# Kernel tuning notes

Measured on AMD Instinct MI355X. Metric: run time of the kernel, lower is better.

The kernel has to match this reference:

```python
import jax, jax.numpy as jnp
import numpy as np

N = 50000        # nodes
E = 800000       # directed edges (before self-loops)
F_IN = 128       # num_features
GAT_DIM = 16     # per-head channels
HEADS = 4
HID = GAT_DIM * HEADS   # 64, concat output of each GATConv
FC = 10 * GAT_DIM       # 160
OUT = 64                # output_dim
NEG_SLOPE = 0.2         # PyG GATConv default


def _gat_conv(x, W, a_src, a_dst, b, src, dst):
    """One PyG-style GATConv (concat=True, self-loops already in src/dst).
    x: [N, Fin], W: [Fin, HEADS*GAT_DIM], a_src/a_dst: [HEADS, GAT_DIM], b: [HEADS*GAT_DIM]."""
    H, C = a_src.shape
    h = (x @ W).reshape(N, H, C)                       # [N,H,C]
    s_src = (h * a_src).sum(-1)                        # [N,H] per-node src score
    s_dst = (h * a_dst).sum(-1)                        # [N,H]
    e = jax.nn.leaky_relu(s_src[src] + s_dst[dst], NEG_SLOPE)  # [Etot,H]
    # segment softmax over incoming edges of each destination node
    m = jax.ops.segment_max(e, dst, num_segments=N)    # [N,H]
    ex = jnp.exp(e - m[dst])
    z = jax.ops.segment_sum(ex, dst, num_segments=N)   # [N,H]
    alpha = ex / (z[dst] + 1e-16)                      # [Etot,H]
    msg = h[src] * alpha[:, :, None]                   # [Etot,H,C]
    out = jax.ops.segment_sum(msg, dst, num_segments=N)
    return out.reshape(N, H * C) + b


def setup_inputs() -> dict:
    key = jax.random.key(0)
    ks = jax.random.split(key, 20)
    sc = 0.05
    inp = {
        "x": jax.random.normal(ks[0], (N, F_IN), dtype=jnp.float32),
        "edge_index": jax.random.randint(ks[1], (2, E), 0, N, dtype=jnp.int32),
        "W0": jax.random.normal(ks[2], (F_IN, HID), dtype=jnp.float32) * sc,
        "as0": jax.random.normal(ks[3], (HEADS, GAT_DIM), dtype=jnp.float32) * sc,
        "ad0": jax.random.normal(ks[4], (HEADS, GAT_DIM), dtype=jnp.float32) * sc,
        "b0": jnp.zeros((HID,), jnp.float32),
        "W1": jax.random.normal(ks[5], (HID, HID), dtype=jnp.float32) * sc,
        "as1": jax.random.normal(ks[6], (HEADS, GAT_DIM), dtype=jnp.float32) * sc,
        "ad1": jax.random.normal(ks[7], (HEADS, GAT_DIM), dtype=jnp.float32) * sc,
        "b1": jnp.zeros((HID,), jnp.float32),
        "W2": jax.random.normal(ks[8], (HID, HID), dtype=jnp.float32) * sc,
        "as2": jax.random.normal(ks[9], (HEADS, GAT_DIM), dtype=jnp.float32) * sc,
        "ad2": jax.random.normal(ks[10], (HEADS, GAT_DIM), dtype=jnp.float32) * sc,
        "b2": jnp.zeros((HID,), jnp.float32),
        "fw1": jax.random.normal(ks[11], (HID, FC), dtype=jnp.float32) * sc,
        "fb1": jnp.zeros((FC,), jnp.float32),
        "fw2": jax.random.normal(ks[12], (FC, OUT), dtype=jnp.float32) * sc,
        "fb2": jnp.zeros((OUT,), jnp.float32),
    }
    return inp


def reference(x, edge_index, W0, as0, ad0, b0, W1, as1, ad1, b1, W2, as2, ad2, b2, fw1, fb1, fw2, fb2):
    loop = jnp.arange(N, dtype=edge_index.dtype)
    src = jnp.concatenate([edge_index[0], loop])   # PyG add_self_loops=True
    dst = jnp.concatenate([edge_index[1], loop])
    h = jax.nn.relu(_gat_conv(x, W0, as0, ad0, b0, src, dst))
    h = jax.nn.relu(_gat_conv(h, W1, as1, ad1, b1, src, dst))
    h = jax.nn.relu(_gat_conv(h, W2, as2, ad2, b2, src, dst))
    h = jax.nn.relu(h @ fw1 + fb1)
    return h @ fw2 + fb2
```

## Files before the change

kernel.cpp:

```cpp
#include <hip/hip_runtime.h>
#include <hip/hip_fp16.h>

#define NN 50000
#define EE 800000
#define ETOT (EE + NN)
#define HIDD 64
#define NHEADS 4
#define FCD 160
#define OUTD 64

#define NBKT 196
#define BSTRIDE 5120
#define CHUNK 4096
#define NEBLK ((ETOT + CHUNK - 1) / CHUNK)
#define NGB   ((NN + 63) / 64)
#define NFC128 ((NN + 127) / 128)


__global__ void k_zero(int* __restrict__ cursor) {
    int t = threadIdx.x;
    if (t < NBKT) cursor[t] = 0;
}

__global__ __launch_bounds__(256) void k_binwrite(const int* __restrict__ ei,
                                                  int* __restrict__ cursor,
                                                  unsigned* __restrict__ binned) {
    __shared__ int hist[NBKT];
    __shared__ int sbase[NBKT];
    __shared__ int cur[NBKT];
    int t = threadIdx.x;
    for (int i = t; i < NBKT; i += 256) hist[i] = 0;
    __syncthreads();
    int base = blockIdx.x * CHUNK;
    for (int k = t; k < CHUNK; k += 256) {
        int i = base + k;
        if (i < ETOT) {
            int dst = (i < EE) ? ei[EE + i] : (i - EE);
            atomicAdd(&hist[dst >> 8], 1);
        }
    }
    __syncthreads();
    for (int b = t; b < NBKT; b += 256) {
        int c = hist[b];
        sbase[b] = b * BSTRIDE + (c ? atomicAdd(&cursor[b], c) : 0);
        cur[b] = 0;
    }
    __syncthreads();
    for (int k = t; k < CHUNK; k += 256) {
        int i = base + k;
        if (i < ETOT) {
            int src, dst;
            if (i < EE) { src = ei[i]; dst = ei[EE + i]; }
            else { src = dst = i - EE; }
            int b = dst >> 8;
            int p = atomicAdd(&cur[b], 1);
            binned[sbase[b] + p] = ((unsigned)src << 8) | (unsigned)(dst & 255);
        }
    }
}

__global__ __launch_bounds__(256) void k_csr_final(const int* __restrict__ cursor,
                                                   const unsigned* __restrict__ binned,
                                                   int* __restrict__ rowbeg,
                                                   int* __restrict__ rowend,
                                                   int* __restrict__ csrc) {
    __shared__ int hist[256];
    __shared__ int cur[256];
    __shared__ int wsum[4];
    int b = blockIdx.x;
    int t = threadIdx.x;
    int s0 = b * BSTRIDE;
    int cnt = cursor[b];
    hist[t] = 0;
    __syncthreads();
    for (int k = t; k < cnt; k += 256) {
        unsigned pr = binned[s0 + k];
        atomicAdd(&hist[pr & 255u], 1);
    }
    __syncthreads();
    int v = hist[t];
    int lane = t & 63, w = t >> 6;
    int x = v;
    #pragma unroll
    for (int off = 1; off < 64; off <<= 1) {
        int y = __shfl_up(x, off);
        if (lane >= off) x += y;
    }
    if (lane == 63) wsum[w] = x;
    __syncthreads();
    int add = 0;
    #pragma unroll
    for (int k = 0; k < 4; k++) add += (k < w) ? wsum[k] : 0;
    int excl = x + add - v;
    int n = (b << 8) + t;
    if (n < NN) {
        rowbeg[n] = s0 + excl;
        rowend[n] = s0 + excl + v;
    }
    cur[t] = s0 + excl;
    __syncthreads();
    for (int k = t; k < cnt; k += 256) {
        unsigned pr = binned[s0 + k];
        int p = atomicAdd(&cur[pr & 255u], 1);
        csrc[p] = (int)(pr >> 8);
    }
}


template<int FIN>
__global__ __launch_bounds__(256) void k_gemm_scores(
        const float* __restrict__ x, const float* __restrict__ W,
        const float* __restrict__ a_src, const float* __restrict__ a_dst,
        __half* __restrict__ h, float* __restrict__ ssrc, float* __restrict__ sdst) {
    __shared__ float wl[64 * 64];
    __shared__ float xt[64][68];
    int t = threadIdx.x;
    int nb = blockIdx.x * 64;
    int qg = t & 15, ng = t >> 4;
    float acc[4][4] = {};
    const float4* wl4 = (const float4*)wl;

    #pragma unroll
    for (int p = 0; p < FIN / 64; p++) {
        if (p) __syncthreads();
        for (int i = t; i < 64 * 64 / 4; i += 256)
            ((float4*)wl)[i] = ((const float4*)W)[p * 1024 + i];
        #pragma unroll
        for (int r = 0; r < 4; r++) {
            int idx = t + r * 256;
            int node = idx & 63, kq = idx >> 6;
            int n = nb + node;
            float4 v = make_float4(0.f, 0.f, 0.f, 0.f);
            if (n < NN) v = *(const float4*)(x + (size_t)n * FIN + p * 64 + kq * 4);
            xt[kq * 4 + 0][node] = v.x;
            xt[kq * 4 + 1][node] = v.y;
            xt[kq * 4 + 2][node] = v.z;
            xt[kq * 4 + 3][node] = v.w;
        }
        __syncthreads();
        #pragma unroll 4
        for (int k = 0; k < 64; k++) {
            float4 wv = wl4[k * 16 + qg];
            float4 xv = *(const float4*)&xt[k][ng * 4];
            acc[0][0] += xv.x * wv.x; acc[0][1] += xv.x * wv.y;
            acc[0][2] += xv.x * wv.z; acc[0][3] += xv.x * wv.w;
            acc[1][0] += xv.y * wv.x; acc[1][1] += xv.y * wv.y;
            acc[1][2] += xv.y * wv.z; acc[1][3] += xv.y * wv.w;
            acc[2][0] += xv.z * wv.x; acc[2][1] += xv.z * wv.y;
            acc[2][2] += xv.z * wv.z; acc[2][3] += xv.z * wv.w;
            acc[3][0] += xv.w * wv.x; acc[3][1] += xv.w * wv.y;
            acc[3][2] += xv.w * wv.z; acc[3][3] += xv.w * wv.w;
        }
    }

    #pragma unroll
    for (int r = 0; r < 4; r++) {
        int n = nb + ng * 4 + r;
        if (n < NN) {
            union { __half2 h2[2]; uint2 u; } pk;
            pk.h2[0] = __floats2half2_rn(acc[r][0], acc[r][1]);
            pk.h2[1] = __floats2half2_rn(acc[r][2], acc[r][3]);
            *(uint2*)(h + (size_t)n * HIDD + qg * 4) = pk.u;
        }
    }

    float as0 = a_src[qg * 4 + 0], as1 = a_src[qg * 4 + 1];
    float as2 = a_src[qg * 4 + 2], as3 = a_src[qg * 4 + 3];
    float ad0 = a_dst[qg * 4 + 0], ad1 = a_dst[qg * 4 + 1];
    float ad2 = a_dst[qg * 4 + 2], ad3 = a_dst[qg * 4 + 3];
    float vs[4], vd[4];
    #pragma unroll
    for (int r = 0; r < 4; r++) {
        vs[r] = acc[r][0] * as0 + acc[r][1] * as1 + acc[r][2] * as2 + acc[r][3] * as3;
        vd[r] = acc[r][0] * ad0 + acc[r][1] * ad1 + acc[r][2] * ad2 + acc[r][3] * ad3;
        vs[r] += __shfl_xor(vs[r], 1); vs[r] += __shfl_xor(vs[r], 2);
        vd[r] += __shfl_xor(vd[r], 1); vd[r] += __shfl_xor(vd[r], 2);
    }
    if ((qg & 3) == 0) {
        int hd = qg >> 2;
        #pragma unroll
        for (int r = 0; r < 4; r++) {
            int n = nb + ng * 4 + r;
            if (n < NN) {
                ssrc[n * NHEADS + hd] = vs[r];
                sdst[n * NHEADS + hd] = vd[r];
            }
        }
    }
}


__global__ __launch_bounds__(512) void k_aggr_gemm(
        const __half* __restrict__ h, const float* __restrict__ ssrc,
        const float* __restrict__ sdst, const int* __restrict__ rowbeg,
        const int* __restrict__ rowend, const int* __restrict__ csrc,
        const float* __restrict__ bias, const float* __restrict__ W,
        const float* __restrict__ a_src, const float* __restrict__ a_dst,
        __half* __restrict__ hout, float* __restrict__ ssrc_o,
        float* __restrict__ sdst_o) {
    __shared__ float wl[64 * 64];
    __shared__ float xt[64][68];
    int t = threadIdx.x;
    int nb = blockIdx.x * 64;

    for (int i = t; i < 64 * 64 / 4; i += 512)
        ((float4*)wl)[i] = ((const float4*)W)[i];

    {
        int wid = t >> 6, lane = t & 63;
        int sub = lane >> 4, c4 = lane & 15, hd = c4 >> 2;
        #pragma unroll 1
        for (int i = 0; i < 8; i++) {
            int nl = wid * 8 + i;
            int n = nb + nl;
            float4 acc = make_float4(0.f, 0.f, 0.f, 0.f);
            float z = 0.f;
            if (n < NN) {
                int beg = rowbeg[n], end = rowend[n];
                float sdh = sdst[n * NHEADS + hd];
                for (int cb = beg; cb < end; cb += 64) {
                    int m = min(64, end - cb);
                    int s_all = (cb + lane < end) ? csrc[cb + lane] : 0;
                    for (int pb = 0; pb < m; pb += 16) {
                        float ssv[4]; uint2 hr[4];
                        #pragma unroll
                        for (int o = 0; o < 4; o++) {
                            int jj = pb + sub * 4 + o;
                            int s = __shfl(s_all, jj);
                            if (jj < m) {
                                ssv[o] = ssrc[s * NHEADS + hd];
                                hr[o] = *(const uint2*)(h + (size_t)s * HIDD + c4 * 4);
                            }
                        }
                        #pragma unroll
                        for (int o = 0; o < 4; o++) {
                            int jj = pb + sub * 4 + o;
                            if (jj < m) {
                                float eh = ssv[o] + sdh;
                                eh = eh > 0.f ? eh : 0.2f * eh;
                                float w = __expf(eh);
                                float2 lo = __half22float2(*(__half2*)&hr[o].x);
                                float2 hi = __half22float2(*(__half2*)&hr[o].y);
                                acc.x += lo.x * w; acc.y += lo.y * w;
                                acc.z += hi.x * w; acc.w += hi.y * w;
                                z += w;
                            }
                        }
                    }
                }
            }
            acc.x += __shfl_xor(acc.x, 16); acc.y += __shfl_xor(acc.y, 16);
            acc.z += __shfl_xor(acc.z, 16); acc.w += __shfl_xor(acc.w, 16);
            z += __shfl_xor(z, 16);
            acc.x += __shfl_xor(acc.x, 32); acc.y += __shfl_xor(acc.y, 32);
            acc.z += __shfl_xor(acc.z, 32); acc.w += __shfl_xor(acc.w, 32);
            z += __shfl_xor(z, 32);
            if (sub == 0) {
                float inv_z = 1.0f / (z + 1e-16f);
                float4 bv = *(const float4*)(bias + c4 * 4);
                float v0 = acc.x * inv_z + bv.x; v0 = v0 > 0.f ? v0 : 0.f;
                float v1 = acc.y * inv_z + bv.y; v1 = v1 > 0.f ? v1 : 0.f;
                float v2 = acc.z * inv_z + bv.z; v2 = v2 > 0.f ? v2 : 0.f;
                float v3 = acc.w * inv_z + bv.w; v3 = v3 > 0.f ? v3 : 0.f;
                if (n >= NN) { v0 = v1 = v2 = v3 = 0.f; }
                xt[c4 * 4 + 0][nl] = v0;
                xt[c4 * 4 + 1][nl] = v1;
                xt[c4 * 4 + 2][nl] = v2;
                xt[c4 * 4 + 3][nl] = v3;
            }
        }
    }
    __syncthreads();

    {
        int qg = t & 15, ng = t >> 4;
        float acc[2][4] = {};
        const float4* wl4 = (const float4*)wl;
        #pragma unroll 4
        for (int k = 0; k < 64; k++) {
            float4 wv = wl4[k * 16 + qg];
            float2 xv = *(const float2*)&xt[k][ng * 2];
            acc[0][0] += xv.x * wv.x; acc[0][1] += xv.x * wv.y;
            acc[0][2] += xv.x * wv.z; acc[0][3] += xv.x * wv.w;
            acc[1][0] += xv.y * wv.x; acc[1][1] += xv.y * wv.y;
            acc[1][2] += xv.y * wv.z; acc[1][3] += xv.y * wv.w;
        }
        #pragma unroll
        for (int r = 0; r < 2; r++) {
            int n = nb + ng * 2 + r;
            if (n < NN) {
                union { __half2 h2[2]; uint2 u; } pk;
                pk.h2[0] = __floats2half2_rn(acc[r][0], acc[r][1]);
                pk.h2[1] = __floats2half2_rn(acc[r][2], acc[r][3]);
                *(uint2*)(hout + (size_t)n * HIDD + qg * 4) = pk.u;
            }
        }
        float as0 = a_src[qg * 4 + 0], as1 = a_src[qg * 4 + 1];
        float as2 = a_src[qg * 4 + 2], as3 = a_src[qg * 4 + 3];
        float ad0 = a_dst[qg * 4 + 0], ad1 = a_dst[qg * 4 + 1];
        float ad2 = a_dst[qg * 4 + 2], ad3 = a_dst[qg * 4 + 3];
        float vs[2], vd[2];
        #pragma unroll
        for (int r = 0; r < 2; r++) {
            vs[r] = acc[r][0] * as0 + acc[r][1] * as1 + acc[r][2] * as2 + acc[r][3] * as3;
            vd[r] = acc[r][0] * ad0 + acc[r][1] * ad1 + acc[r][2] * ad2 + acc[r][3] * ad3;
            vs[r] += __shfl_xor(vs[r], 1); vs[r] += __shfl_xor(vs[r], 2);
            vd[r] += __shfl_xor(vd[r], 1); vd[r] += __shfl_xor(vd[r], 2);
        }
        if ((qg & 3) == 0) {
            int hd = qg >> 2;
            #pragma unroll
            for (int r = 0; r < 2; r++) {
                int n = nb + ng * 2 + r;
                if (n < NN) {
                    ssrc_o[n * NHEADS + hd] = vs[r];
                    sdst_o[n * NHEADS + hd] = vd[r];
                }
            }
        }
    }
}


__global__ __launch_bounds__(256) void k_aggr(
        const __half* __restrict__ h, const float* __restrict__ ssrc,
        const float* __restrict__ sdst, const int* __restrict__ rowbeg,
        const int* __restrict__ rowend,
        const int* __restrict__ csrc, const float* __restrict__ bias,
        __half* __restrict__ out) {
    int wid  = threadIdx.x >> 6;
    int lane = threadIdx.x & 63;
    int n = blockIdx.x * 4 + wid;
    int sub = lane >> 4;
    int c4  = lane & 15;
    int hd  = c4 >> 2;
    int beg = rowbeg[n], end = rowend[n];
    float sdh = sdst[n * NHEADS + hd];

    float4 acc = make_float4(0.f, 0.f, 0.f, 0.f);
    float z = 0.f;
    for (int cb = beg; cb < end; cb += 64) {
        int m = min(64, end - cb);
        int s_all = (cb + lane < end) ? csrc[cb + lane] : 0;
        for (int pb = 0; pb < m; pb += 16) {
            float ssv[4]; uint2 hr[4];
            #pragma unroll
            for (int o = 0; o < 4; o++) {
                int jj = pb + sub * 4 + o;
                int s = __shfl(s_all, jj);
                if (jj < m) {
                    ssv[o] = ssrc[s * NHEADS + hd];
                    hr[o] = *(const uint2*)(h + (size_t)s * HIDD + c4 * 4);
                }
            }
            #pragma unroll
            for (int o = 0; o < 4; o++) {
                int jj = pb + sub * 4 + o;
                if (jj < m) {
                    float eh = ssv[o] + sdh;
                    eh = eh > 0.f ? eh : 0.2f * eh;
                    float w = __expf(eh);
                    float2 lo = __half22float2(*(__half2*)&hr[o].x);
                    float2 hi = __half22float2(*(__half2*)&hr[o].y);
                    acc.x += lo.x * w; acc.y += lo.y * w;
                    acc.z += hi.x * w; acc.w += hi.y * w;
                    z += w;
                }
            }
        }
    }
    acc.x += __shfl_xor(acc.x, 16); acc.y += __shfl_xor(acc.y, 16);
    acc.z += __shfl_xor(acc.z, 16); acc.w += __shfl_xor(acc.w, 16);
    z += __shfl_xor(z, 16);
    acc.x += __shfl_xor(acc.x, 32); acc.y += __shfl_xor(acc.y, 32);
    acc.z += __shfl_xor(acc.z, 32); acc.w += __shfl_xor(acc.w, 32);
    z += __shfl_xor(z, 32);

    if (sub == 0) {
        float inv_z = 1.0f / (z + 1e-16f);
        float4 bv = *(const float4*)(bias + c4 * 4);
        float v0 = acc.x * inv_z + bv.x; v0 = v0 > 0.f ? v0 : 0.f;
        float v1 = acc.y * inv_z + bv.y; v1 = v1 > 0.f ? v1 : 0.f;
        float v2 = acc.z * inv_z + bv.z; v2 = v2 > 0.f ? v2 : 0.f;
        float v3 = acc.w * inv_z + bv.w; v3 = v3 > 0.f ? v3 : 0.f;
        union { __half2 h2[2]; uint2 u; } pk;
        pk.h2[0] = __floats2half2_rn(v0, v1);
        pk.h2[1] = __floats2half2_rn(v2, v3);
        *(uint2*)(out + (size_t)n * HIDD + c4 * 4) = pk.u;
    }
}


__global__ __launch_bounds__(256) void k_fc_fused(const __half* __restrict__ x,
        const float* __restrict__ W1, const float* __restrict__ b1,
        const float* __restrict__ W2, const float* __restrict__ b2,
        float* __restrict__ out) {
    __shared__ float wl[32 * 160];
    __shared__ __half xt[32][132];
    __shared__ __half y[160][136];
    int t = threadIdx.x;
    int nb = blockIdx.x * 128;
    const float4* wl4 = (const float4*)wl;

    {
        int qg = t & 7, ng = t >> 3;
        float acc[4][5][4] = {};
        #pragma unroll
        for (int p = 0; p < 2; p++) {
            if (p) __syncthreads();
            for (int i = t; i < 32 * 160 / 4; i += 256)
                ((float4*)wl)[i] = ((const float4*)W1)[p * 32 * 40 + i];
            #pragma unroll
            for (int r = 0; r < 4; r++) {
                int idx = t + r * 256;
                int node = idx & 127, kq = idx >> 7;
                int n = nb + node;
                uint2 v = make_uint2(0u, 0u);
                if (n < NN) v = *(const uint2*)(x + (size_t)n * 64 + p * 32 + kq * 4);
                __half2 h0 = *(__half2*)&v.x;
                __half2 h1 = *(__half2*)&v.y;
                xt[kq * 4 + 0][node] = __low2half(h0);
                xt[kq * 4 + 1][node] = __high2half(h0);
                xt[kq * 4 + 2][node] = __low2half(h1);
                xt[kq * 4 + 3][node] = __high2half(h1);
            }
            __syncthreads();
            #pragma unroll 4
            for (int k = 0; k < 32; k++) {
                uint2 xr = *(const uint2*)&xt[k][ng * 4];
                float2 x01 = __half22float2(*(__half2*)&xr.x);
                float2 x23 = __half22float2(*(__half2*)&xr.y);
                #pragma unroll
                for (int i = 0; i < 5; i++) {
                    float4 wv = wl4[k * 40 + qg + 8 * i];
                    acc[0][i][0] += x01.x * wv.x; acc[0][i][1] += x01.x * wv.y;
                    acc[0][i][2] += x01.x * wv.z; acc[0][i][3] += x01.x * wv.w;
                    acc[1][i][0] += x01.y * wv.x; acc[1][i][1] += x01.y * wv.y;
                    acc[1][i][2] += x01.y * wv.z; acc[1][i][3] += x01.y * wv.w;
                    acc[2][i][0] += x23.x * wv.x; acc[2][i][1] += x23.x * wv.y;
                    acc[2][i][2] += x23.x * wv.z; acc[2][i][3] += x23.x * wv.w;
                    acc[3][i][0] += x23.y * wv.x; acc[3][i][1] += x23.y * wv.y;
                    acc[3][i][2] += x23.y * wv.z; acc[3][i][3] += x23.y * wv.w;
                }
            }
        }
        #pragma unroll
        for (int i = 0; i < 5; i++) {
            int j0 = (qg + 8 * i) * 4;
            float4 bv = *(const float4*)(b1 + j0);
            #pragma unroll
            for (int r = 0; r < 4; r++) {
                int node = ng * 4 + r;
                float v0 = acc[r][i][0] + bv.x; v0 = v0 > 0.f ? v0 : 0.f;
                float v1 = acc[r][i][1] + bv.y; v1 = v1 > 0.f ? v1 : 0.f;
                float v2 = acc[r][i][2] + bv.z; v2 = v2 > 0.f ? v2 : 0.f;
                float v3 = acc[r][i][3] + bv.w; v3 = v3 > 0.f ? v3 : 0.f;
                y[j0 + 0][node] = __float2half_rn(v0);
                y[j0 + 1][node] = __float2half_rn(v1);
                y[j0 + 2][node] = __float2half_rn(v2);
                y[j0 + 3][node] = __float2half_rn(v3);
            }
        }
    }
    __syncthreads();

    {
        int qg = t & 15, ng = t >> 4;
        float acc[8][4] = {};
        #pragma unroll
        for (int p = 0; p < 2; p++) {
            if (p) __syncthreads();
            for (int i = t; i < 80 * 64 / 4; i += 256)
                ((float4*)wl)[i] = ((const float4*)W2)[p * 80 * 16 + i];
            __syncthreads();
            #pragma unroll 2
            for (int k = 0; k < 80; k++) {
                float4 wv = wl4[k * 16 + qg];
                uint4 yr = *(const uint4*)&y[p * 80 + k][ng * 8];
                float2 f0 = __half22float2(*(__half2*)&yr.x);
                float2 f1 = __half22float2(*(__half2*)&yr.y);
                float2 f2 = __half22float2(*(__half2*)&yr.z);
                float2 f3 = __half22float2(*(__half2*)&yr.w);
                acc[0][0] += f0.x * wv.x; acc[0][1] += f0.x * wv.y;
                acc[0][2] += f0.x * wv.z; acc[0][3] += f0.x * wv.w;
                acc[1][0] += f0.y * wv.x; acc[1][1] += f0.y * wv.y;
                acc[1][2] += f0.y * wv.z; acc[1][3] += f0.y * wv.w;
                acc[2][0] += f1.x * wv.x; acc[2][1] += f1.x * wv.y;
                acc[2][2] += f1.x * wv.z; acc[2][3] += f1.x * wv.w;
                acc[3][0] += f1.y * wv.x; acc[3][1] += f1.y * wv.y;
                acc[3][2] += f1.y * wv.z; acc[3][3] += f1.y * wv.w;
                acc[4][0] += f2.x * wv.x; acc[4][1] += f2.x * wv.y;
                acc[4][2] += f2.x * wv.z; acc[4][3] += f2.x * wv.w;
                acc[5][0] += f2.y * wv.x; acc[5][1] += f2.y * wv.y;
                acc[5][2] += f2.y * wv.z; acc[5][3] += f2.y * wv.w;
                acc[6][0] += f3.x * wv.x; acc[6][1] += f3.x * wv.y;
                acc[6][2] += f3.x * wv.z; acc[6][3] += f3.x * wv.w;
                acc[7][0] += f3.y * wv.x; acc[7][1] += f3.y * wv.y;
                acc[7][2] += f3.y * wv.z; acc[7][3] += f3.y * wv.w;
            }
        }
        int j0 = qg * 4;
        float4 bv = *(const float4*)(b2 + j0);
        #pragma unroll
        for (int r = 0; r < 8; r++) {
            int n = nb + ng * 8 + r;
            if (n < NN) {
                float4 o;
                o.x = acc[r][0] + bv.x; o.y = acc[r][1] + bv.y;
                o.z = acc[r][2] + bv.z; o.w = acc[r][3] + bv.w;
                *(float4*)(out + (size_t)n * 64 + j0) = o;
            }
        }
    }
}


extern "C" void kernel_launch(void* const* d_in, const int* in_sizes, int n_in,
                              void* d_out, int out_size, void* d_ws, size_t ws_size,
                              hipStream_t stream) {
    const float* x   = (const float*)d_in[0];
    const int*   ei  = (const int*)d_in[1];
    const float* W0  = (const float*)d_in[2];
    const float* as0 = (const float*)d_in[3];
    const float* ad0 = (const float*)d_in[4];
    const float* b0  = (const float*)d_in[5];
    const float* W1  = (const float*)d_in[6];
    const float* as1 = (const float*)d_in[7];
    const float* ad1 = (const float*)d_in[8];
    const float* b1  = (const float*)d_in[9];
    const float* W2  = (const float*)d_in[10];
    const float* as2 = (const float*)d_in[11];
    const float* ad2 = (const float*)d_in[12];
    const float* b2  = (const float*)d_in[13];
    const float* fw1 = (const float*)d_in[14];
    const float* fb1 = (const float*)d_in[15];
    const float* fw2 = (const float*)d_in[16];
    const float* fb2 = (const float*)d_in[17];

    float* ws = (float*)d_ws;
    __half* hA  = (__half*)ws;
    __half* hB  = (__half*)(ws + (size_t)NN * 32);
    float* sAsrc = ws + (size_t)NN * 64;
    float* sAdst = sAsrc + (size_t)NN * NHEADS;
    float* sBsrc = sAdst + (size_t)NN * NHEADS;
    float* sBdst = sBsrc + (size_t)NN * NHEADS;
    float* actf  = sBdst + (size_t)NN * NHEADS;
    __half* act  = (__half*)actf;
    float* scr   = actf + (size_t)NN * 32;
    unsigned* binned = (unsigned*)scr;
    int*   csrc   = (int*)scr + 1100000;
    int*   rowbeg = (int*)scr + 2200000;
    int*   rowend = (int*)scr + 2300000;
    int*   cursor = (int*)scr + 2400000;

    k_zero<<<1, 256, 0, stream>>>(cursor);
    k_binwrite<<<NEBLK, 256, 0, stream>>>(ei, cursor, binned);
    k_csr_final<<<NBKT, 256, 0, stream>>>(cursor, binned, rowbeg, rowend, csrc);

    k_gemm_scores<128><<<NGB, 256, 0, stream>>>(x, W0, as0, ad0, hA, sAsrc, sAdst);
    k_aggr_gemm<<<NGB, 512, 0, stream>>>(hA, sAsrc, sAdst, rowbeg, rowend, csrc,
                                         b0, W1, as1, ad1, hB, sBsrc, sBdst);
    k_aggr_gemm<<<NGB, 512, 0, stream>>>(hB, sBsrc, sBdst, rowbeg, rowend, csrc,
                                         b1, W2, as2, ad2, hA, sAsrc, sAdst);
    k_aggr<<<NN / 4, 256, 0, stream>>>(hA, sAsrc, sAdst, rowbeg, rowend, csrc, b2, act);

    k_fc_fused<<<NFC128, 256, 0, stream>>>(act, fw1, fb1, fw2, fb2, (float*)d_out);
}
```

Measured before the change: 197.5 us.

## Use packed fp16 dot2 instructions in fused FC head with pre-packed weights

Adds a small kernel that converts the FC weights to pairs of fp16 values packed along K. The fused FC kernel now computes with v_dot2 (fp16 pairs, fp32 accumulate) instead of converting activations to fp32 and doing scalar FMAs. The node tile shrinks from 128 to 64 and the weight staging is no longer split into two passes, which cuts register use and raises block count. Weights are now rounded to fp16, so accuracy drops slightly, and one extra small launch is added.

```diff
diff --git a/kernel.cpp b/kernel.cpp
--- a/kernel.cpp
+++ b/kernel.cpp
@@ -14,7 +14,26 @@
 #define CHUNK 4096
 #define NEBLK ((ETOT + CHUNK - 1) / CHUNK)
 #define NGB   ((NN + 63) / 64)
-#define NFC128 ((NN + 127) / 128)
+
+typedef _Float16 hf2 __attribute__((ext_vector_type(2)));
+
+static __device__ __forceinline__ float fdot2f(unsigned a, unsigned b, float c) {
+#if defined(__has_builtin)
+#if __has_builtin(__builtin_amdgcn_fdot2)
+    union { unsigned u; hf2 h; } ua, ub;
+    ua.u = a; ub.u = b;
+    return __builtin_amdgcn_fdot2(ua.h, ub.h, c, false);
+#else
+    __half2 ha = *(__half2*)&a, hb = *(__half2*)&b;
+    float2 fa = __half22float2(ha), fb = __half22float2(hb);
+    return c + fa.x * fb.x + fa.y * fb.y;
+#endif
+#else
+    __half2 ha = *(__half2*)&a, hb = *(__half2*)&b;
+    float2 fa = __half22float2(ha), fb = __half22float2(hb);
+    return c + fa.x * fb.x + fa.y * fb.y;
+#endif
+}
 
 
 __global__ void k_zero(int* __restrict__ cursor) {
@@ -103,6 +122,24 @@
         unsigned pr = binned[s0 + k];
         int p = atomicAdd(&cur[pr & 255u], 1);
         csrc[p] = (int)(pr >> 8);
+    }
+}
+
+
+__global__ __launch_bounds__(256) void k_packw(const float* __restrict__ W1,
+                                               const float* __restrict__ W2,
+                                               unsigned* __restrict__ W1p,
+                                               unsigned* __restrict__ W2p) {
+    int i = blockIdx.x * 256 + threadIdx.x;
+    if (i < 32 * 160) {
+        int k2 = i / 160, j = i - k2 * 160;
+        __half2 p = __floats2half2_rn(W1[(2 * k2) * 160 + j], W1[(2 * k2 + 1) * 160 + j]);
+        W1p[i] = *(unsigned*)&p;
+    }
+    if (i < 80 * 64) {
+        int k2 = i / 64, j = i - k2 * 64;
+        __half2 p = __floats2half2_rn(W2[(2 * k2) * 64 + j], W2[(2 * k2 + 1) * 64 + j]);
+        W2p[i] = *(unsigned*)&p;
     }
 }
 
@@ -392,56 +429,47 @@
 
 
 __global__ __launch_bounds__(256) void k_fc_fused(const __half* __restrict__ x,
-        const float* __restrict__ W1, const float* __restrict__ b1,
-        const float* __restrict__ W2, const float* __restrict__ b2,
+        const unsigned* __restrict__ W1p, const float* __restrict__ b1,
+        const unsigned* __restrict__ W2p, const float* __restrict__ b2,
         float* __restrict__ out) {
-    __shared__ float wl[32 * 160];
-    __shared__ __half xt[32][132];
-    __shared__ __half y[160][136];
+    __shared__ unsigned wl[5120];
+    __shared__ unsigned xt2[32][68];
+    __shared__ unsigned y2[80][68];
     int t = threadIdx.x;
-    int nb = blockIdx.x * 128;
-    const float4* wl4 = (const float4*)wl;
+    int nb = blockIdx.x * 64;
+    const uint4* wl4 = (const uint4*)wl;
+
+    for (int i = t; i < 5120 / 4; i += 256)
+        ((uint4*)wl)[i] = ((const uint4*)W1p)[i];
+    #pragma unroll
+    for (int r = 0; r < 4; r++) {
+        int idx = t + r * 256;
+        int node = idx & 63, kq = idx >> 6;
+        int n = nb + node;
+        uint2 v = make_uint2(0u, 0u);
+        if (n < NN) v = ((const uint2*)(x + (size_t)n * 64))[kq];
+        xt2[kq * 2 + 0][node] = v.x;
+        xt2[kq * 2 + 1][node] = v.y;
+    }
+    __syncthreads();
 
     {
         int qg = t & 7, ng = t >> 3;
-        float acc[4][5][4] = {};
-        #pragma unroll
-        for (int p = 0; p < 2; p++) {
-            if (p) __syncthreads();
-            for (int i = t; i < 32 * 160 / 4; i += 256)
-                ((float4*)wl)[i] = ((const float4*)W1)[p * 32 * 40 + i];
+        float acc[2][5][4] = {};
+        #pragma unroll 2
+        for (int k2 = 0; k2 < 32; k2++) {
+            uint2 xv = *(const uint2*)&xt2[k2][ng * 2];
             #pragma unroll
-            for (int r = 0; r < 4; r++) {
-                int idx = t + r * 256;
-                int node = idx & 127, kq = idx >> 7;
-                int n = nb + node;
-                uint2 v = make_uint2(0u, 0u);
-                if (n < NN) v = *(const uint2*)(x + (size_t)n * 64 + p * 32 + kq * 4);
-                __half2 h0 = *(__half2*)&v.x;
-                __half2 h1 = *(__half2*)&v.y;
-                xt[kq * 4 + 0][node] = __low2half(h0);
-                xt[kq * 4 + 1][node] = __high2half(h0);
-                xt[kq * 4 + 2][node] = __low2half(h1);
-                xt[kq * 4 + 3][node] = __high2half(h1);
-            }
-            __syncthreads();
-            #pragma unroll 4
-            for (int k = 0; k < 32; k++) {
-                uint2 xr = *(const uint2*)&xt[k][ng * 4];
-                float2 x01 = __half22float2(*(__half2*)&xr.x);
-                float2 x23 = __half22float2(*(__half2*)&xr.y);
-                #pragma unroll
-                for (int i = 0; i < 5; i++) {
-                    float4 wv = wl4[k * 40 + qg + 8 * i];
-                    acc[0][i][0] += x01.x * wv.x; acc[0][i][1] += x01.x * wv.y;
-                    acc[0][i][2] += x01.x * wv.z; acc[0][i][3] += x01.x * wv.w;
-                    acc[1][i][0] += x01.y * wv.x; acc[1][i][1] += x01.y * wv.y;
-                    acc[1][i][2] += x01.y * wv.z; acc[1][i][3] += x01.y * wv.w;
-                    acc[2][i][0] += x23.x * wv.x; acc[2][i][1] += x23.x * wv.y;
-                    acc[2][i][2] += x23.x * wv.z; acc[2][i][3] += x23.x * wv.w;
-                    acc[3][i][0] += x23.y * wv.x; acc[3][i][1] += x23.y * wv.y;
-                    acc[3][i][2] += x23.y * wv.z; acc[3][i][3] += x23.y * wv.w;
-                }
+            for (int i = 0; i < 5; i++) {
+                uint4 wv = wl4[k2 * 40 + qg + 8 * i];
+                acc[0][i][0] = fdot2f(xv.x, wv.x, acc[0][i][0]);
+                acc[0][i][1] = fdot2f(xv.x, wv.y, acc[0][i][1]);
+                acc[0][i][2] = fdot2f(xv.x, wv.z, acc[0][i][2]);
+                acc[0][i][3] = fdot2f(xv.x, wv.w, acc[0][i][3]);
+                acc[1][i][0] = fdot2f(xv.y, wv.x, acc[1][i][0]);
+                acc[1][i][1] = fdot2f(xv.y, wv.y, acc[1][i][1]);
+                acc[1][i][2] = fdot2f(xv.y, wv.z, acc[1][i][2]);
+                acc[1][i][3] = fdot2f(xv.y, wv.w, acc[1][i][3]);
             }
         }
         #pragma unroll
@@ -449,61 +477,54 @@
             int j0 = (qg + 8 * i) * 4;
             float4 bv = *(const float4*)(b1 + j0);
             #pragma unroll
-            for (int r = 0; r < 4; r++) {
-                int node = ng * 4 + r;
+            for (int r = 0; r < 2; r++) {
+                int node = ng * 2 + r;
                 float v0 = acc[r][i][0] + bv.x; v0 = v0 > 0.f ? v0 : 0.f;
                 float v1 = acc[r][i][1] + bv.y; v1 = v1 > 0.f ? v1 : 0.f;
                 float v2 = acc[r][i][2] + bv.z; v2 = v2 > 0.f ? v2 : 0.f;
                 float v3 = acc[r][i][3] + bv.w; v3 = v3 > 0.f ? v3 : 0.f;
-                y[j0 + 0][node] = __float2half_rn(v0);
-                y[j0 + 1][node] = __float2half_rn(v1);
-                y[j0 + 2][node] = __float2half_rn(v2);
-                y[j0 + 3][node] = __float2half_rn(v3);
-            }
-        }
-    }
+                __half2 p0 = __floats2half2_rn(v0, v1);
+                __half2 p1 = __floats2half2_rn(v2, v3);
+                y2[(qg + 8 * i) * 2 + 0][node] = *(unsigned*)&p0;
+                y2[(qg + 8 * i) * 2 + 1][node] = *(unsigned*)&p1;
+            }
+        }
+    }
+    __syncthreads();
+
+    for (int i = t; i < 5120 / 4; i += 256)
+        ((uint4*)wl)[i] = ((const uint4*)W2p)[i];
     __syncthreads();
 
     {
         int qg = t & 15, ng = t >> 4;
-        float acc[8][4] = {};
-        #pragma unroll
-        for (int p = 0; p < 2; p++) {
-            if (p) __syncthreads();
-            for (int i = t; i < 80 * 64 / 4; i += 256)
-                ((float4*)wl)[i] = ((const float4*)W2)[p * 80 * 16 + i];
-            __syncthreads();
-            #pragma unroll 2
-            for (int k = 0; k < 80; k++) {
-                float4 wv = wl4[k * 16 + qg];
-                uint4 yr = *(const uint4*)&y[p * 80 + k][ng * 8];
-                float2 f0 = __half22float2(*(__half2*)&yr.x);
-                float2 f1 = __half22float2(*(__half2*)&yr.y);
-                float2 f2 = __half22float2(*(__half2*)&yr.z);
-                float2 f3 = __half22float2(*(__half2*)&yr.w);
-                acc[0][0] += f0.x * wv.x; acc[0][1] += f0.x * wv.y;
-                acc[0][2] += f0.x * wv.z; acc[0][3] += f0.x * wv.w;
-                acc[1][0] += f0.y * wv.x; acc[1][1] += f0.y * wv.y;
-                acc[1][2] += f0.y * wv.z; acc[1][3] += f0.y * wv.w;
-                acc[2][0] += f1.x * wv.x; acc[2][1] += f1.x * wv.y;
-                acc[2][2] += f1.x * wv.z; acc[2][3] += f1.x * wv.w;
-                acc[3][0] += f1.y * wv.x; acc[3][1] += f1.y * wv.y;
-                acc[3][2] += f1.y * wv.z; acc[3][3] += f1.y * wv.w;
-                acc[4][0] += f2.x * wv.x; acc[4][1] += f2.x * wv.y;
-                acc[4][2] += f2.x * wv.z; acc[4][3] += f2.x * wv.w;
-                acc[5][0] += f2.y * wv.x; acc[5][1] += f2.y * wv.y;
-                acc[5][2] += f2.y * wv.z; acc[5][3] += f2.y * wv.w;
-                acc[6][0] += f3.x * wv.x; acc[6][1] += f3.x * wv.y;
-                acc[6][2] += f3.x * wv.z; acc[6][3] += f3.x * wv.w;
-                acc[7][0] += f3.y * wv.x; acc[7][1] += f3.y * wv.y;
-                acc[7][2] += f3.y * wv.z; acc[7][3] += f3.y * wv.w;
-            }
+        float acc[4][4] = {};
+        #pragma unroll 2
+        for (int k2 = 0; k2 < 80; k2++) {
+            uint4 wv = wl4[k2 * 16 + qg];
+            uint4 yv = *(const uint4*)&y2[k2][ng * 4];
+            acc[0][0] = fdot2f(yv.x, wv.x, acc[0][0]);
+            acc[0][1] = fdot2f(yv.x, wv.y, acc[0][1]);
+            acc[0][2] = fdot2f(yv.x, wv.z, acc[0][2]);
+            acc[0][3] = fdot2f(yv.x, wv.w, acc[0][3]);
+            acc[1][0] = fdot2f(yv.y, wv.x, acc[1][0]);
+            acc[1][1] = fdot2f(yv.y, wv.y, acc[1][1]);
+            acc[1][2] = fdot2f(yv.y, wv.z, acc[1][2]);
+            acc[1][3] = fdot2f(yv.y, wv.w, acc[1][3]);
+            acc[2][0] = fdot2f(yv.z, wv.x, acc[2][0]);
+            acc[2][1] = fdot2f(yv.z, wv.y, acc[2][1]);
+            acc[2][2] = fdot2f(yv.z, wv.z, acc[2][2]);
+            acc[2][3] = fdot2f(yv.z, wv.w, acc[2][3]);
+            acc[3][0] = fdot2f(yv.w, wv.x, acc[3][0]);
+            acc[3][1] = fdot2f(yv.w, wv.y, acc[3][1]);
+            acc[3][2] = fdot2f(yv.w, wv.z, acc[3][2]);
+            acc[3][3] = fdot2f(yv.w, wv.w, acc[3][3]);
         }
         int j0 = qg * 4;
         float4 bv = *(const float4*)(b2 + j0);
         #pragma unroll
-        for (int r = 0; r < 8; r++) {
-            int n = nb + ng * 8 + r;
+        for (int r = 0; r < 4; r++) {
+            int n = nb + ng * 4 + r;
             if (n < NN) {
                 float4 o;
                 o.x = acc[r][0] + bv.x; o.y = acc[r][1] + bv.y;
@@ -552,8 +573,11 @@
     int*   rowbeg = (int*)scr + 2200000;
     int*   rowend = (int*)scr + 2300000;
     int*   cursor = (int*)scr + 2400000;
+    unsigned* W1p = (unsigned*)scr + 2410000;
+    unsigned* W2p = (unsigned*)scr + 2420000;
 
     k_zero<<<1, 256, 0, stream>>>(cursor);
+    k_packw<<<20, 256, 0, stream>>>(fw1, fw2, W1p, W2p);
     k_binwrite<<<NEBLK, 256, 0, stream>>>(ei, cursor, binned);
     k_csr_final<<<NBKT, 256, 0, stream>>>(cursor, binned, rowbeg, rowend, csrc);
 
@@ -564,5 +588,5 @@
                                          b1, W2, as2, ad2, hA, sAsrc, sAdst);
     k_aggr<<<NN / 4, 256, 0, stream>>>(hA, sAsrc, sAdst, rowbeg, rowend, csrc, b2, act);
 
-    k_fc_fused<<<NFC128, 256, 0, stream>>>(act, fw1, fb1, fw2, fb2, (float*)d_out);
-}
+    k_fc_fused<<<NGB, 256, 0, stream>>>(act, W1p, fb1, W2p, fb2, (float*)d_out);
+}
```

Result: faster. 188.9 us (-4.4%).
